# Optimization experiments

Hardware: AMD Instinct MI355X
Metric: run time of the kernel (lower is better)

Reference implementation:

```python
import jax, jax.numpy as jnp
import numpy as np

K = 256           # number of selected features (init kwarg k)
NUM_SAMPLES = 8   # init kwarg num_samples
BATCH = 256
NUM_FEATURES = 20000


def setup_inputs() -> dict:
    key = jax.random.key(0)
    logits = jax.random.normal(key, (BATCH, NUM_FEATURES, 1), dtype=jnp.float32)
    return {"logits": logits, "tau": 1, "training": 0}


def reference(logits, tau, training):
    # Eval branch of SubsetLayer.forward (training=False).
    # logits: [B, N, 1]
    B, N, _ = logits.shape
    scores = logits[..., 0]                       # [B, N]
    _, idx = jax.lax.top_k(scores, K)             # idx: [B, K]
    # k-hot mask built directly by scatter (equivalent to one_hot(...).sum(1))
    khot = jnp.zeros((B, N), dtype=jnp.float32)
    khot = khot.at[jnp.arange(B)[:, None], idx].set(1.0)  # [B, N]
    # unsqueeze(0).unsqueeze(-1).expand(num_samples, -1, -1, -1)
    out = jnp.broadcast_to(khot[None, :, :, None], (NUM_SAMPLES, B, N, 1))
    return out
```

## Files before the change

kernel.cpp:

```cpp
#include <hip/hip_runtime.h>

#define BATCH   256
#define NFEAT   20000
#define NVEC    (NFEAT / 4)
#define KSEL    256
#define NSAMP   8
#define CAP     2048
#define RANKC   512

typedef unsigned long long u64;
typedef float    __attribute__((ext_vector_type(4))) f32x4;
typedef unsigned __attribute__((ext_vector_type(4))) u32x4;

__device__ __forceinline__ unsigned fmap(float f) {
    unsigned u = __float_as_uint(f);
    return (u & 0x80000000u) ? ~u : (u | 0x80000000u);
}

__device__ __forceinline__ void select_bin_wave0(const unsigned* hist, int nbins, int w,
                                                 int* s_d, int* s_w, int lane) {
    for (int base = nbins - 1; base >= 0; base -= 64) {
        int bin = base - lane;
        unsigned c = (bin >= 0) ? hist[bin] : 0u;
        unsigned p = c;
#pragma unroll
        for (int off = 1; off < 64; off <<= 1) {
            unsigned t = __shfl_up(p, off);
            if (lane >= off) p += t;
        }
        unsigned long long m = __ballot(p >= (unsigned)w);
        if (m) {
            int l = __ffsll(m) - 1;
            if (lane == l) { *s_d = bin; *s_w = w - (int)(p - c); }
            return;
        }
        w -= (int)__shfl(p, 63);
    }
    if (lane == 0) { *s_d = 0; *s_w = 1; }
}

__device__ __forceinline__ void pick64(const unsigned* arr, int w, int lane,
                                       int* s_idx, int* s_w) {
    unsigned c = arr[63 - lane];
    unsigned p = c;
#pragma unroll
    for (int off = 1; off < 64; off <<= 1) {
        unsigned t = __shfl_up(p, off);
        if (lane >= off) p += t;
    }
    unsigned long long m = __ballot(p >= (unsigned)w);
    if (m) {
        int l = __ffsll(m) - 1;
        if (lane == l) { *s_idx = 63 - l; *s_w = w - (int)(p - c); }
    } else if (lane == 0) { *s_idx = 0; *s_w = 1; }
}

__global__ __launch_bounds__(1024) void topk_fused(const float* __restrict__ logits,
                                                   float* __restrict__ out) {
    const int b = blockIdx.x, tid = threadIdx.x;
    const int lane = tid & 63, wave = tid >> 6;
    const float4* __restrict__ row4 = (const float4*)(logits + (size_t)b * NFEAT);

    __shared__ __align__(16) unsigned key[NFEAT];
    __shared__ unsigned hist[4096];
    __shared__ u64 candA[CAP];
    __shared__ u64 candB[CAP];
    __shared__ unsigned csum[64];
    __shared__ int s_d, s_w;
    __shared__ unsigned s_cnt;
    __shared__ u64 s_thr;
    __shared__ int s_run, s_cut, s_wc[16];

    u32x4* key4 = (u32x4*)key;

    for (int i = tid; i < 4096; i += 1024) hist[i] = 0;
    __syncthreads();
    for (int i = tid; i < NVEC; i += 1024) {
        float4 v = row4[i];
        unsigned k0 = fmap(v.x), k1 = fmap(v.y), k2 = fmap(v.z), k3 = fmap(v.w);
        u32x4 kv; kv.x = k0; kv.y = k1; kv.z = k2; kv.w = k3;
        key4[i] = kv;
        atomicAdd(&hist[k0 >> 20], 1u);
        atomicAdd(&hist[k1 >> 20], 1u);
        atomicAdd(&hist[k2 >> 20], 1u);
        atomicAdd(&hist[k3 >> 20], 1u);
    }
    __syncthreads();

    unsigned keypref; int w; int shift = 20;
    {
#pragma unroll
        for (int j = 0; j < 4; ++j) {
            const int c = wave * 4 + j;
            unsigned v = hist[c * 64 + lane];
#pragma unroll
            for (int off = 32; off; off >>= 1) v += __shfl_down(v, off);
            if (lane == 0) csum[c] = v;
        }
        __syncthreads();
        if (wave == 0) pick64(csum, KSEL, lane, &s_d, &s_w);
        __syncthreads();
        const int chunk = s_d; const int w0 = s_w;
        if (wave == 0) pick64(&hist[chunk * 64], w0, lane, &s_d, &s_w);
        __syncthreads();
        keypref = (unsigned)(chunk * 64 + s_d);
        w = s_w;
    }
    unsigned cnt = hist[keypref];
    __syncthreads();

    while (cnt > CAP && shift > 0) {
        const int nb = (shift >= 12) ? 12 : shift;
        const int nsh = shift - nb;
        const unsigned mask = (1u << nb) - 1u;
        for (int i = tid; i < (1 << nb); i += 1024) hist[i] = 0;
        __syncthreads();
        for (int i = tid; i < NFEAT; i += 1024) {
            unsigned k = key[i];
            if ((k >> shift) == keypref) atomicAdd(&hist[(k >> nsh) & mask], 1u);
        }
        __syncthreads();
        if (wave == 0) select_bin_wave0(hist, 1 << nb, w, &s_d, &s_w, lane);
        __syncthreads();
        keypref = (keypref << nb) | (unsigned)s_d;
        w = s_w;
        shift = nsh;
        cnt = hist[s_d];
        __syncthreads();
    }

    if (tid == 0) s_cnt = 0;
    __syncthreads();
    for (int i = tid; i < NFEAT; i += 1024) {
        unsigned k = key[i];
        if ((k >> shift) == keypref) {
            unsigned p = atomicAdd(&s_cnt, 1u);
            if (p < CAP) candA[p] = ((u64)k << 32) | (unsigned)~i;
        }
    }
    __syncthreads();
    unsigned C = s_cnt;

    if (C <= CAP) {
        u64* src = candA; u64* dst = candB;
        int pshift = 32 + shift;
        while (C > RANKC && pshift > 0) {
            const int nb = (pshift >= 12) ? 12 : pshift;
            const int nsh = pshift - nb;
            const unsigned mask = (1u << nb) - 1u;
            for (int i = tid; i < (1 << nb); i += 1024) hist[i] = 0;
            __syncthreads();
            for (int i = tid; i < (int)C; i += 1024)
                atomicAdd(&hist[(unsigned)(src[i] >> nsh) & mask], 1u);
            __syncthreads();
            if (wave == 0) select_bin_wave0(hist, 1 << nb, w, &s_d, &s_w, lane);
            __syncthreads();
            const unsigned d = (unsigned)s_d;
            w = s_w;
            if (tid == 0) s_cnt = 0;
            __syncthreads();
            for (int i = tid; i < (int)C; i += 1024) {
                u64 c = src[i];
                if (((unsigned)(c >> nsh) & mask) == d) {
                    unsigned p = atomicAdd(&s_cnt, 1u);
                    dst[p] = c;
                }
            }
            __syncthreads();
            C = s_cnt;
            pshift = nsh;
            u64* t = src; src = dst; dst = t;
            __syncthreads();
        }
        for (int i = tid; i < (int)C; i += 1024) {
            u64 ci = src[i];
            int cgt = 0;
            for (int j = 0; j < (int)C; ++j) cgt += (src[j] > ci) ? 1 : 0;
            if (cgt == w - 1) s_thr = ci;
        }
        __syncthreads();
    } else {
        if (tid == 0) { s_run = 0; s_cut = 0; }
        __syncthreads();
        for (int base = 0; base < NFEAT; base += 1024) {
            const int i = base + tid;
            const bool eq = (i < NFEAT) && (key[i] == keypref);
            const unsigned long long bal = __ballot(eq);
            if (lane == 0) s_wc[wave] = __popcll(bal);
            __syncthreads();
            int off = s_run;
            for (int x = 0; x < wave; ++x) off += s_wc[x];
            const int rank = off + __popcll(bal & ((lane == 0) ? 0ull : ((1ull << lane) - 1ull)));
            if (eq && rank == w - 1) s_cut = i;
            __syncthreads();
            if (tid == 0) { int t = 0; for (int x = 0; x < 16; ++x) t += s_wc[x]; s_run += t; }
            __syncthreads();
            if (s_run >= w) break;
        }
        if (tid == 0) s_thr = ((u64)keypref << 32) | (unsigned)~s_cut;
        __syncthreads();
    }

    const u64 thr = s_thr;
    const size_t rowoff = (size_t)b * NFEAT;
    for (int i = tid; i < NVEC; i += 1024) {
        const u32x4 k = key4[i];
        const int n = i * 4;
        f32x4 m;
        m.x = ((((u64)k.x << 32) | (unsigned)~(n + 0)) >= thr) ? 1.0f : 0.0f;
        m.y = ((((u64)k.y << 32) | (unsigned)~(n + 1)) >= thr) ? 1.0f : 0.0f;
        m.z = ((((u64)k.z << 32) | (unsigned)~(n + 2)) >= thr) ? 1.0f : 0.0f;
        m.w = ((((u64)k.w << 32) | (unsigned)~(n + 3)) >= thr) ? 1.0f : 0.0f;
#pragma unroll
        for (int s = 0; s < NSAMP; ++s) {
            *reinterpret_cast<f32x4*>(out + (size_t)s * BATCH * NFEAT + rowoff + n) = m;
        }
    }
}

extern "C" void kernel_launch(void* const* d_in, const int* in_sizes, int n_in,
                              void* d_out, int out_size, void* d_ws, size_t ws_size,
                              hipStream_t stream) {
    const float* logits = (const float*)d_in[0];
    float* out = (float*)d_out;
    (void)d_ws; (void)ws_size;

    topk_fused<<<BATCH, 1024, 0, stream>>>(logits, out);
}
```

Before: 42.44 us.

## Keep row keys in registers instead of LDS and drop candidate refinement passes

Each thread now loads its five float4s up front and keeps the mapped keys in registers for the whole kernel, removing the 80KB LDS key array and re-reads of it during histogram refinement, candidate gathering and mask writing. The candidate-narrowing loop (RANKC refinement with ping-pong buffers) is removed, so the final O(C^2) rank step runs on up to CAP candidates. Candidate gathering is merged into the refinement loop. Lower LDS use may allow more blocks per CU, at the cost of higher register pressure and a possibly costlier quadratic rank when many candidates remain.

Result: faster. 36.63 us (-13.7%).

```diff
diff --git a/kernel.cpp b/kernel.cpp
--- a/kernel.cpp
+++ b/kernel.cpp
@@ -6,11 +6,9 @@
 #define KSEL    256
 #define NSAMP   8
 #define CAP     2048
-#define RANKC   512
 
 typedef unsigned long long u64;
-typedef float    __attribute__((ext_vector_type(4))) f32x4;
-typedef unsigned __attribute__((ext_vector_type(4))) u32x4;
+typedef float __attribute__((ext_vector_type(4))) f32x4;
 
 __device__ __forceinline__ unsigned fmap(float f) {
     unsigned u = __float_as_uint(f);
@@ -61,137 +59,144 @@
     const int lane = tid & 63, wave = tid >> 6;
     const float4* __restrict__ row4 = (const float4*)(logits + (size_t)b * NFEAT);
 
-    __shared__ __align__(16) unsigned key[NFEAT];
     __shared__ unsigned hist[4096];
-    __shared__ u64 candA[CAP];
-    __shared__ u64 candB[CAP];
+    __shared__ u64 cand[CAP];
     __shared__ unsigned csum[64];
     __shared__ int s_d, s_w;
     __shared__ unsigned s_cnt;
     __shared__ u64 s_thr;
     __shared__ int s_run, s_cut, s_wc[16];
 
-    u32x4* key4 = (u32x4*)key;
-
-    for (int i = tid; i < 4096; i += 1024) hist[i] = 0;
+    float4 v[5];
+#pragma unroll
+    for (int j = 0; j < 5; ++j) {
+        const int i4 = tid + j * 1024;
+        v[j] = row4[(i4 < NVEC) ? i4 : (NVEC - 1)];
+    }
+#pragma unroll
+    for (int j = 0; j < 4; ++j) hist[tid + j * 1024] = 0;
     __syncthreads();
-    for (int i = tid; i < NVEC; i += 1024) {
-        float4 v = row4[i];
-        unsigned k0 = fmap(v.x), k1 = fmap(v.y), k2 = fmap(v.z), k3 = fmap(v.w);
-        u32x4 kv; kv.x = k0; kv.y = k1; kv.z = k2; kv.w = k3;
-        key4[i] = kv;
-        atomicAdd(&hist[k0 >> 20], 1u);
-        atomicAdd(&hist[k1 >> 20], 1u);
-        atomicAdd(&hist[k2 >> 20], 1u);
-        atomicAdd(&hist[k3 >> 20], 1u);
+
+    unsigned kk[5][4];
+#pragma unroll
+    for (int j = 0; j < 5; ++j) {
+        kk[j][0] = fmap(v[j].x); kk[j][1] = fmap(v[j].y);
+        kk[j][2] = fmap(v[j].z); kk[j][3] = fmap(v[j].w);
+    }
+#pragma unroll
+    for (int j = 0; j < 4; ++j) {
+#pragma unroll
+        for (int e = 0; e < 4; ++e) atomicAdd(&hist[kk[j][e] >> 20], 1u);
+    }
+    if (tid + 4096 < NVEC) {
+#pragma unroll
+        for (int e = 0; e < 4; ++e) atomicAdd(&hist[kk[4][e] >> 20], 1u);
     }
     __syncthreads();
 
-    unsigned keypref; int w; int shift = 20;
+    unsigned keypref; int w;
     {
 #pragma unroll
         for (int j = 0; j < 4; ++j) {
             const int c = wave * 4 + j;
-            unsigned v = hist[c * 64 + lane];
-#pragma unroll
-            for (int off = 32; off; off >>= 1) v += __shfl_down(v, off);
-            if (lane == 0) csum[c] = v;
+            unsigned x = hist[c * 64 + lane];
+#pragma unroll
+            for (int off = 32; off; off >>= 1) x += __shfl_down(x, off);
+            if (lane == 0) csum[c] = x;
         }
         __syncthreads();
         if (wave == 0) pick64(csum, KSEL, lane, &s_d, &s_w);
         __syncthreads();
         const int chunk = s_d; const int w0 = s_w;
         if (wave == 0) pick64(&hist[chunk * 64], w0, lane, &s_d, &s_w);
+        if (tid == 0) s_cnt = 0;
         __syncthreads();
         keypref = (unsigned)(chunk * 64 + s_d);
         w = s_w;
     }
-    unsigned cnt = hist[keypref];
-    __syncthreads();
-
-    while (cnt > CAP && shift > 0) {
+    int shift = 20;
+
+    unsigned C;
+    for (;;) {
+#pragma unroll
+        for (int j = 0; j < 5; ++j) {
+            const int i4 = tid + j * 1024;
+            if (i4 < NVEC) {
+#pragma unroll
+                for (int e = 0; e < 4; ++e) {
+                    const unsigned k = kk[j][e];
+                    if ((k >> shift) == keypref) {
+                        unsigned p = atomicAdd(&s_cnt, 1u);
+                        if (p < CAP) cand[p] = ((u64)k << 32) | (unsigned)~(4 * i4 + e);
+                    }
+                }
+            }
+        }
+        __syncthreads();
+        C = s_cnt;
+        if (C <= CAP || shift == 0) break;
+
         const int nb = (shift >= 12) ? 12 : shift;
         const int nsh = shift - nb;
-        const unsigned mask = (1u << nb) - 1u;
         for (int i = tid; i < (1 << nb); i += 1024) hist[i] = 0;
         __syncthreads();
-        for (int i = tid; i < NFEAT; i += 1024) {
-            unsigned k = key[i];
-            if ((k >> shift) == keypref) atomicAdd(&hist[(k >> nsh) & mask], 1u);
+#pragma unroll
+        for (int j = 0; j < 5; ++j) {
+            const int i4 = tid + j * 1024;
+            if (i4 < NVEC) {
+#pragma unroll
+                for (int e = 0; e < 4; ++e) {
+                    const unsigned k = kk[j][e];
+                    if ((k >> shift) == keypref)
+                        atomicAdd(&hist[(k >> nsh) & ((1u << nb) - 1u)], 1u);
+                }
+            }
         }
         __syncthreads();
         if (wave == 0) select_bin_wave0(hist, 1 << nb, w, &s_d, &s_w, lane);
+        if (tid == 0) s_cnt = 0;
         __syncthreads();
         keypref = (keypref << nb) | (unsigned)s_d;
         w = s_w;
         shift = nsh;
-        cnt = hist[s_d];
-        __syncthreads();
-    }
-
-    if (tid == 0) s_cnt = 0;
-    __syncthreads();
-    for (int i = tid; i < NFEAT; i += 1024) {
-        unsigned k = key[i];
-        if ((k >> shift) == keypref) {
-            unsigned p = atomicAdd(&s_cnt, 1u);
-            if (p < CAP) candA[p] = ((u64)k << 32) | (unsigned)~i;
-        }
-    }
-    __syncthreads();
-    unsigned C = s_cnt;
+    }
 
     if (C <= CAP) {
-        u64* src = candA; u64* dst = candB;
-        int pshift = 32 + shift;
-        while (C > RANKC && pshift > 0) {
-            const int nb = (pshift >= 12) ? 12 : pshift;
-            const int nsh = pshift - nb;
-            const unsigned mask = (1u << nb) - 1u;
-            for (int i = tid; i < (1 << nb); i += 1024) hist[i] = 0;
-            __syncthreads();
-            for (int i = tid; i < (int)C; i += 1024)
-                atomicAdd(&hist[(unsigned)(src[i] >> nsh) & mask], 1u);
-            __syncthreads();
-            if (wave == 0) select_bin_wave0(hist, 1 << nb, w, &s_d, &s_w, lane);
-            __syncthreads();
-            const unsigned d = (unsigned)s_d;
-            w = s_w;
-            if (tid == 0) s_cnt = 0;
-            __syncthreads();
-            for (int i = tid; i < (int)C; i += 1024) {
-                u64 c = src[i];
-                if (((unsigned)(c >> nsh) & mask) == d) {
-                    unsigned p = atomicAdd(&s_cnt, 1u);
-                    dst[p] = c;
-                }
-            }
-            __syncthreads();
-            C = s_cnt;
-            pshift = nsh;
-            u64* t = src; src = dst; dst = t;
-            __syncthreads();
-        }
         for (int i = tid; i < (int)C; i += 1024) {
-            u64 ci = src[i];
+            const u64 ci = cand[i];
             int cgt = 0;
-            for (int j = 0; j < (int)C; ++j) cgt += (src[j] > ci) ? 1 : 0;
+            for (int j = 0; j < (int)C; ++j) cgt += (cand[j] > ci) ? 1 : 0;
             if (cgt == w - 1) s_thr = ci;
         }
         __syncthreads();
     } else {
         if (tid == 0) { s_run = 0; s_cut = 0; }
         __syncthreads();
-        for (int base = 0; base < NFEAT; base += 1024) {
-            const int i = base + tid;
-            const bool eq = (i < NFEAT) && (key[i] == keypref);
-            const unsigned long long bal = __ballot(eq);
-            if (lane == 0) s_wc[wave] = __popcll(bal);
+#pragma unroll 1
+        for (int j = 0; j < 5; ++j) {
+            const int i4 = tid + j * 1024;
+            bool eq[4];
+            int cnt4 = 0;
+#pragma unroll
+            for (int e = 0; e < 4; ++e) {
+                eq[e] = (i4 < NVEC) && (kk[j][e] == keypref);
+                cnt4 += eq[e] ? 1 : 0;
+            }
+            unsigned p = (unsigned)cnt4;
+#pragma unroll
+            for (int off = 1; off < 64; off <<= 1) {
+                unsigned t = __shfl_up(p, off);
+                if (lane >= off) p += t;
+            }
+            const unsigned excl = p - (unsigned)cnt4;
+            if (lane == 63) s_wc[wave] = (int)p;
             __syncthreads();
-            int off = s_run;
-            for (int x = 0; x < wave; ++x) off += s_wc[x];
-            const int rank = off + __popcll(bal & ((lane == 0) ? 0ull : ((1ull << lane) - 1ull)));
-            if (eq && rank == w - 1) s_cut = i;
+            int off0 = s_run + (int)excl;
+            for (int x = 0; x < wave; ++x) off0 += s_wc[x];
+#pragma unroll
+            for (int e = 0; e < 4; ++e) {
+                if (eq[e]) { if (off0 == w - 1) s_cut = 4 * i4 + e; ++off0; }
+            }
             __syncthreads();
             if (tid == 0) { int t = 0; for (int x = 0; x < 16; ++x) t += s_wc[x]; s_run += t; }
             __syncthreads();
@@ -202,18 +207,25 @@
     }
 
     const u64 thr = s_thr;
-    const size_t rowoff = (size_t)b * NFEAT;
-    for (int i = tid; i < NVEC; i += 1024) {
-        const u32x4 k = key4[i];
-        const int n = i * 4;
-        f32x4 m;
-        m.x = ((((u64)k.x << 32) | (unsigned)~(n + 0)) >= thr) ? 1.0f : 0.0f;
-        m.y = ((((u64)k.y << 32) | (unsigned)~(n + 1)) >= thr) ? 1.0f : 0.0f;
-        m.z = ((((u64)k.z << 32) | (unsigned)~(n + 2)) >= thr) ? 1.0f : 0.0f;
-        m.w = ((((u64)k.w << 32) | (unsigned)~(n + 3)) >= thr) ? 1.0f : 0.0f;
-#pragma unroll
-        for (int s = 0; s < NSAMP; ++s) {
-            *reinterpret_cast<f32x4*>(out + (size_t)s * BATCH * NFEAT + rowoff + n) = m;
+    const unsigned thr_k = (unsigned)(thr >> 32);
+    const unsigned thr_l = (unsigned)thr;
+    float* const outb = out + (size_t)b * NFEAT;
+#pragma unroll
+    for (int j = 0; j < 5; ++j) {
+        const int i4 = tid + j * 1024;
+        if (i4 < NVEC) {
+            const int n = 4 * i4;
+            f32x4 m;
+#pragma unroll
+            for (int e = 0; e < 4; ++e) {
+                const unsigned k = kk[j][e];
+                const bool sel = (k > thr_k) || (k == thr_k && (unsigned)~(n + e) >= thr_l);
+                m[e] = sel ? 1.0f : 0.0f;
+            }
+#pragma unroll
+            for (int s = 0; s < NSAMP; ++s) {
+                *reinterpret_cast<f32x4*>(outb + (size_t)s * ((size_t)BATCH * NFEAT) + n) = m;
+            }
         }
     }
 }
```
